# Performance work log

Measured on AMD Instinct MI355X. Metric: run time of the kernel, lower is better.

Reference implementation:

```python
import jax, jax.numpy as jnp
import numpy as np

B, S, D_IN, H, L = 32, 1024, 128, 256, 2
ND = 2  # bidirectional


def setup_inputs() -> dict:
    key = jax.random.key(0)
    ks = iter(jax.random.split(key, 40))

    def p(shape, scale=0.05):
        return jax.random.normal(next(ks), shape, dtype=jnp.float32) * scale

    inp = {"x": jax.random.normal(next(ks), (B, S, D_IN), dtype=jnp.float32)}
    dims_in = [D_IN, H * ND]
    for l in range(L):
        for tag in ("f", "b"):
            inp[f"w_ih_l{l}{tag}"] = p((4 * H, dims_in[l]))
            inp[f"w_hh_l{l}{tag}"] = p((4 * H, H))
            inp[f"b_l{l}{tag}"] = p((4 * H,))  # b_ih + b_hh fused (identical math)
    inp["attn_w"] = p((H * ND,))   # nn.Linear(2H, 1) weight
    inp["attn_b"] = p((1,))
    inp["head_w"] = p((D_IN, H * ND))  # forecasting head: Linear(2H, input_dim)
    inp["head_b"] = p((D_IN,))
    return inp


def _lstm_dir(x, w_ih, w_hh, b, reverse):
    """Single-direction LSTM over [B,S,F] -> [B,S,H]. PyTorch gate order i,f,g,o."""
    Bb = x.shape[0]
    Hh = w_hh.shape[1]
    # Precompute input projections once: [S,B,4H]
    xp = jnp.einsum('bsi,gi->sbg', x, w_ih) + b
    if reverse:
        xp = xp[::-1]
    h0 = jnp.zeros((Bb, Hh), x.dtype)
    c0 = jnp.zeros((Bb, Hh), x.dtype)

    def step(carry, gx):
        h, c = carry
        g = gx + h @ w_hh.T
        i, f, gg, o = jnp.split(g, 4, axis=-1)
        c = jax.nn.sigmoid(f) * c + jax.nn.sigmoid(i) * jnp.tanh(gg)
        h = jax.nn.sigmoid(o) * jnp.tanh(c)
        return (h, c), h

    _, hs = jax.lax.scan(step, (h0, c0), xp)
    if reverse:
        hs = hs[::-1]
    return jnp.swapaxes(hs, 0, 1)  # [B,S,H]


def reference(x,
              w_ih_l0f, w_hh_l0f, b_l0f, w_ih_l0b, w_hh_l0b, b_l0b,
              w_ih_l1f, w_hh_l1f, b_l1f, w_ih_l1b, w_hh_l1b, b_l1b,
              attn_w, attn_b, head_w, head_b):
    h = x
    layers = [((w_ih_l0f, w_hh_l0f, b_l0f), (w_ih_l0b, w_hh_l0b, b_l0b)),
              ((w_ih_l1f, w_hh_l1f, b_l1f), (w_ih_l1b, w_hh_l1b, b_l1b))]
    for fw, bw in layers:
        hf = _lstm_dir(h, *fw, False)
        hb = _lstm_dir(h, *bw, True)
        h = jnp.concatenate([hf, hb], axis=-1)  # [B,S,2H]; dropout off (eval)
    # Prefix attention pooling: original recomputes softmax over output[:, :i+1]
    # for every i. Equivalently (softmax is shift-invariant per prefix):
    # context_i = cumsum(e * h)_i / cumsum(e)_i with e = exp(s - max(s)).
    s = h @ attn_w + attn_b[0]                      # [B,S] attention scores
    e = jnp.exp(s - jnp.max(s, axis=1, keepdims=True))
    num = jnp.cumsum(e[..., None] * h, axis=1)      # [B,S,2H]
    den = jnp.cumsum(e, axis=1)[..., None]          # [B,S,1]
    context = num / den                             # [B,S,2H]
    forecasts = context @ head_w.T + head_b         # [B,S,D_IN]
    return forecasts
```

## Files before the change

### kernel.cpp

```cpp
#include <hip/hip_runtime.h>

typedef unsigned short ushort_t;
typedef unsigned int uint_t;
typedef unsigned long long u64;
typedef __attribute__((ext_vector_type(8))) short short8;
typedef __attribute__((ext_vector_type(4))) float floatx4;

#define S_LEN 1024
#define BATCH 32
#define HDIM  256
#define GDIM  1024
#define DIN   128
#define TAG_BASE 0xC0FFE000u

__device__ __forceinline__ float bf2f(ushort_t u) { return __uint_as_float(((unsigned)u) << 16); }
__device__ __forceinline__ float bf2fs(short s)   { return __uint_as_float(((unsigned)(unsigned short)s) << 16); }
__device__ __forceinline__ ushort_t f2bf(float f) {
  unsigned u = __float_as_uint(f);
  unsigned r = (u + 0x7fffu + ((u >> 16) & 1u)) >> 16;
  return (ushort_t)r;
}
__device__ __forceinline__ float sigf(float x) { return 1.f / (1.f + __expf(-x)); }
__device__ __forceinline__ float tanh_f(float x) {
  float ax = fabsf(x);
  float e = __expf(2.f * ax);
  float r = 1.f - 2.f / (e + 1.f);
  return x < 0.f ? -r : r;
}

__device__ __forceinline__ void load_lds16(const void* g, void* l) {
  __builtin_amdgcn_global_load_lds((const __attribute__((address_space(1))) unsigned int*)g,
                                   (__attribute__((address_space(3))) unsigned int*)l, 16, 0, 0);
}

__global__ __launch_bounds__(256) void gemm_bf16(
    const ushort_t* __restrict__ A, const ushort_t* __restrict__ Bw,
    const float* __restrict__ bias, void* __restrict__ Cout,
    int M, int N, int K, int mode)
{
  __shared__ __align__(16) ushort_t As[128 * 64];
  __shared__ __align__(16) ushort_t Bs[128 * 64];
  const int tid = threadIdx.x;
  const int lane = tid & 63, wid = tid >> 6;
  const int wm = wid >> 1, wn = wid & 1;
  const int bm = blockIdx.y, bn = blockIdx.x;
  const int l15 = lane & 15, q4 = lane >> 4;

  const int r  = tid >> 3;
  const int c8 = tid & 7;
  const int g8 = c8 ^ (r & 7);

  floatx4 zero4 = {0.f, 0.f, 0.f, 0.f};
  floatx4 acc[4][4];
#pragma unroll
  for (int mt = 0; mt < 4; ++mt)
#pragma unroll
    for (int nt = 0; nt < 4; ++nt) acc[mt][nt] = zero4;

  for (int k0 = 0; k0 < K; k0 += 64) {
    __syncthreads();
#pragma unroll
    for (int p = 0; p < 4; ++p) {
      int row = p * 32 + r;
      load_lds16(A + (size_t)(bm * 128 + row) * K + k0 + g8 * 8, (void*)(As + p * 2048 + wid * 512));
      load_lds16(Bw + (size_t)(bn * 128 + row) * K + k0 + g8 * 8, (void*)(Bs + p * 2048 + wid * 512));
    }
    __syncthreads();
#pragma unroll
    for (int ks = 0; ks < 2; ++ks) {
      const int kk = ks * 4 + q4;
      short8 af[4], bf[4];
#pragma unroll
      for (int mt = 0; mt < 4; ++mt) {
        int row = wm * 64 + mt * 16 + l15;
        af[mt] = *(const short8*)(As + row * 64 + ((kk ^ (row & 7)) << 3));
      }
#pragma unroll
      for (int nt = 0; nt < 4; ++nt) {
        int row = wn * 64 + nt * 16 + l15;
        bf[nt] = *(const short8*)(Bs + row * 64 + ((kk ^ (row & 7)) << 3));
      }
#pragma unroll
      for (int mt = 0; mt < 4; ++mt)
#pragma unroll
        for (int nt = 0; nt < 4; ++nt)
          acc[mt][nt] = __builtin_amdgcn_mfma_f32_16x16x32_bf16(af[mt], bf[nt], acc[mt][nt], 0, 0, 0);
    }
  }

#pragma unroll
  for (int mt = 0; mt < 4; ++mt)
#pragma unroll
    for (int nt = 0; nt < 4; ++nt)
#pragma unroll
      for (int rr = 0; rr < 4; ++rr) {
        int m = bm * 128 + wm * 64 + mt * 16 + q4 * 4 + rr;
        int n = bn * 128 + wn * 64 + nt * 16 + l15;
        float v = acc[mt][nt][rr] + bias[n];
        if (mode == 0) {
          ((ushort_t*)Cout)[(size_t)m * N + n] = f2bf(v);
        } else if (mode == 1) {
          int t = m >> 5, b = m & 31;
          ((float*)Cout)[(size_t)b * (S_LEN * DIN) + t * DIN + n] = v;
        } else {
          int t = m >> 5, b = m & 31;
          ((ushort_t*)Cout)[(size_t)t * (N * 32) + n * 32 + b] = f2bf(v);
        }
      }
}

__global__ __launch_bounds__(256) void lstm_layer(
    const ushort_t* __restrict__ xpf, const ushort_t* __restrict__ xpb,
    const ushort_t* __restrict__ whhf, const ushort_t* __restrict__ whhb,
    ushort_t* __restrict__ hout, u64* __restrict__ comm)
{
  const int bx = blockIdx.x;
  const int dir = bx & 1, j = bx >> 1;

  const ushort_t* xp  = dir ? xpb : xpf;
  const ushort_t* whh = dir ? whhb : whhf;
  u64* commd = comm + (size_t)dir * 8192;
  const int hoff = dir * 256;

  __shared__ __align__(16) ushort_t hbuf[32 * 264];
  __shared__ __align__(16) float stage[32 * 132];

  const int tid = threadIdx.x, lane = tid & 63, w = tid >> 6;
  const int l15 = lane & 15, q4 = lane >> 4;

  short8 Bf[2][8];
#pragma unroll
  for (int tl = 0; tl < 2; ++tl) {
    int grow = w * 256 + j * 32 + tl * 16 + l15;
#pragma unroll
    for (int ks = 0; ks < 8; ++ks)
      Bf[tl][ks] = *(const short8*)(whh + (size_t)grow * 256 + ks * 32 + q4 * 8);
  }

  for (int i = tid; i < 32 * 132; i += 256) ((uint_t*)hbuf)[i] = 0u;

  float cst[4] = {0.f, 0.f, 0.f, 0.f};

  u64 xr64[2][2];
  auto ldxp = [&](int tt) {
#pragma unroll
    for (int mt = 0; mt < 2; ++mt)
#pragma unroll
      for (int tl = 0; tl < 2; ++tl) {
        int g = w * 256 + j * 32 + tl * 16 + l15;
        xr64[mt][tl] = *(const u64*)(xp + (size_t)tt * (GDIM * BATCH) + (size_t)g * 32 + mt * 16 + q4 * 4);
      }
  };

  const int cb  = tid >> 3;
  const int cg0 = tid & 7;
  const int bb  = tid >> 3;
  const int c4  = (tid & 7) * 4;

  ldxp((dir == 0) ? 0 : 1023);
  __syncthreads();

  for (int sc = 0; sc < 1024; ++sc) {
    const int tcur  = (dir == 0) ? sc : 1023 - sc;
    const int tnext = (dir == 0) ? (sc < 1023 ? sc + 1 : 1023) : (sc < 1023 ? 1022 - sc : 0);

    floatx4 acc[2][2];
#pragma unroll
    for (int mt = 0; mt < 2; ++mt)
#pragma unroll
      for (int tl = 0; tl < 2; ++tl) {
        u64 v = xr64[mt][tl];
#pragma unroll
        for (int rr = 0; rr < 4; ++rr)
          acc[mt][tl][rr] = bf2f((ushort_t)(v >> (16 * rr)));
      }

    ldxp(tnext);

    if (sc > 0) {
      const unsigned want = TAG_BASE + (unsigned)sc;
      const u64* rbuf = commd + (size_t)(sc & 1) * 4096 + (size_t)cb * 128 + cg0 * 16;
      u64 v[16];
      for (;;) {
#pragma unroll
        for (int k = 0; k < 16; ++k)
          v[k] = __hip_atomic_load(rbuf + k, __ATOMIC_RELAXED, __HIP_MEMORY_SCOPE_AGENT);
        unsigned bad = 0;
#pragma unroll
        for (int k = 0; k < 16; ++k) bad |= ((unsigned)(v[k] >> 32)) ^ want;
        if (bad == 0) break;
      }
#pragma unroll
      for (int k2 = 0; k2 < 8; ++k2) {
        u64 d = (u64)(uint_t)v[2 * k2] | ((u64)(uint_t)v[2 * k2 + 1] << 32);
        *(u64*)(hbuf + cb * 264 + cg0 * 32 + k2 * 4) = d;
      }
    }
    __syncthreads();

#pragma unroll
    for (int ks = 0; ks < 8; ++ks) {
      short8 a0 = *(const short8*)(hbuf + l15 * 264 + ks * 32 + q4 * 8);
      short8 a1 = *(const short8*)(hbuf + (16 + l15) * 264 + ks * 32 + q4 * 8);
      acc[0][0] = __builtin_amdgcn_mfma_f32_16x16x32_bf16(a0, Bf[0][ks], acc[0][0], 0, 0, 0);
      acc[0][1] = __builtin_amdgcn_mfma_f32_16x16x32_bf16(a0, Bf[1][ks], acc[0][1], 0, 0, 0);
      acc[1][0] = __builtin_amdgcn_mfma_f32_16x16x32_bf16(a1, Bf[0][ks], acc[1][0], 0, 0, 0);
      acc[1][1] = __builtin_amdgcn_mfma_f32_16x16x32_bf16(a1, Bf[1][ks], acc[1][1], 0, 0, 0);
    }

#pragma unroll
    for (int mt = 0; mt < 2; ++mt)
#pragma unroll
      for (int tl = 0; tl < 2; ++tl)
#pragma unroll
        for (int rr = 0; rr < 4; ++rr)
          stage[(mt * 16 + q4 * 4 + rr) * 132 + w * 32 + tl * 16 + l15] = acc[mt][tl][rr];
    __syncthreads();

    float hv4[4];
#pragma unroll
    for (int i = 0; i < 4; ++i) {
      float gi = stage[bb * 132 +       c4 + i];
      float gf = stage[bb * 132 + 32  + c4 + i];
      float gg = stage[bb * 132 + 64  + c4 + i];
      float go = stage[bb * 132 + 96  + c4 + i];
      float c = sigf(gf) * cst[i] + sigf(gi) * tanh_f(gg);
      cst[i] = c;
      hv4[i] = sigf(go) * tanh_f(c);
    }
    u64 pv = (u64)f2bf(hv4[0]) | ((u64)f2bf(hv4[1]) << 16) |
             ((u64)f2bf(hv4[2]) << 32) | ((u64)f2bf(hv4[3]) << 48);

    {
      u64* wbuf = commd + (size_t)((sc + 1) & 1) * 4096;
      const u64 tagw = ((u64)(TAG_BASE + (unsigned)(sc + 1))) << 32;
      size_t wi = (size_t)bb * 128 + j * 16 + (c4 >> 1);
      __hip_atomic_store(wbuf + wi,     tagw | (uint_t)pv,         __ATOMIC_RELAXED, __HIP_MEMORY_SCOPE_AGENT);
      __hip_atomic_store(wbuf + wi + 1, tagw | (uint_t)(pv >> 32), __ATOMIC_RELAXED, __HIP_MEMORY_SCOPE_AGENT);
      *(u64*)(hout + (size_t)tcur * (BATCH * 512) + bb * 512 + hoff + j * 32 + c4) = pv;
    }
    __syncthreads();
  }
}

__global__ __launch_bounds__(256) void attn_scores(
    const ushort_t* __restrict__ h1, const float* __restrict__ attn_w,
    const float* __restrict__ attn_b, float* __restrict__ e_out)
{
  const int b = blockIdx.x;
  __shared__ float sbuf[1024];
  __shared__ float red[4];
  const int tid = threadIdx.x, lane = tid & 63, w = tid >> 6;

  float wreg[8];
#pragma unroll
  for (int i = 0; i < 8; ++i) wreg[i] = attn_w[lane * 8 + i];

  for (int t = w; t < 1024; t += 4) {
    short8 hv = *(const short8*)(h1 + (size_t)t * (BATCH * 512) + b * 512 + lane * 8);
    float dot = 0.f;
#pragma unroll
    for (int i = 0; i < 8; ++i) dot += bf2fs(hv[i]) * wreg[i];
#pragma unroll
    for (int off = 32; off; off >>= 1) dot += __shfl_xor(dot, off);
    if (lane == 0) sbuf[t] = dot + attn_b[0];
  }
  __syncthreads();
  float m = -1e30f;
  for (int t = tid; t < 1024; t += 256) m = fmaxf(m, sbuf[t]);
#pragma unroll
  for (int off = 32; off; off >>= 1) m = fmaxf(m, __shfl_xor(m, off));
  if (lane == 0) red[w] = m;
  __syncthreads();
  float mm = fmaxf(fmaxf(red[0], red[1]), fmaxf(red[2], red[3]));
  for (int t = tid; t < 1024; t += 256) e_out[b * 1024 + t] = __expf(sbuf[t] - mm);
}

__global__ __launch_bounds__(256) void attn_ctx(
    const ushort_t* __restrict__ h1, const float* __restrict__ e_in, ushort_t* __restrict__ ctx)
{
  const int b = blockIdx.x >> 1, half = blockIdx.x & 1;
  const int c = half * 256 + threadIdx.x;
  float num = 0.f, den = 0.f;
  const ushort_t* hp = h1 + b * 512 + c;
  ushort_t* cp = ctx + b * 512 + c;
  const float* ep = e_in + b * 1024;
#pragma unroll 4
  for (int t = 0; t < 1024; ++t) {
    float ev = ep[t];
    float hv = bf2f(hp[(size_t)t * (BATCH * 512)]);
    num += ev * hv;
    den += ev;
    cp[(size_t)t * (BATCH * 512)] = f2bf(num / den);
  }
}

__global__ void castw(const float* __restrict__ in, ushort_t* __restrict__ out, int n) {
  int i = blockIdx.x * 256 + threadIdx.x;
  if (i < n) out[i] = f2bf(in[i]);
}
__global__ void castx(const float* __restrict__ x, ushort_t* __restrict__ xt) {
  int i = blockIdx.x * 256 + threadIdx.x;
  int dcol = i & 127;
  int m = i >> 7;
  int b = m & 31, s = m >> 5;
  xt[i] = f2bf(x[(size_t)b * (S_LEN * DIN) + s * DIN + dcol]);
}

extern "C" void kernel_launch(void* const* d_in, const int* in_sizes, int n_in,
                              void* d_out, int out_size, void* d_ws, size_t ws_size,
                              hipStream_t stream)
{
  const float* x     = (const float*)d_in[0];
  const float* wih0f = (const float*)d_in[1];
  const float* whh0f = (const float*)d_in[2];
  const float* b0f   = (const float*)d_in[3];
  const float* wih0b = (const float*)d_in[4];
  const float* whh0b = (const float*)d_in[5];
  const float* b0b   = (const float*)d_in[6];
  const float* wih1f = (const float*)d_in[7];
  const float* whh1f = (const float*)d_in[8];
  const float* b1f   = (const float*)d_in[9];
  const float* wih1b = (const float*)d_in[10];
  const float* whh1b = (const float*)d_in[11];
  const float* b1b   = (const float*)d_in[12];
  const float* attw  = (const float*)d_in[13];
  const float* attb  = (const float*)d_in[14];
  const float* headw = (const float*)d_in[15];
  const float* headb = (const float*)d_in[16];
  float* out = (float*)d_out;

  char* p = (char*)d_ws;
  auto alloc = [&](size_t bytes) {
    char* r = p;
    p += (bytes + 511) & ~(size_t)511;
    return r;
  };
  u64* comm0      = (u64*)alloc(16384 * 8);
  u64* comm1      = (u64*)alloc(16384 * 8);
  ushort_t* xt    = (ushort_t*)alloc((size_t)32768 * 128 * 2);
  ushort_t* cwih0f = (ushort_t*)alloc(131072 * 2);
  ushort_t* cwih0b = (ushort_t*)alloc(131072 * 2);
  ushort_t* cwhh0f = (ushort_t*)alloc(262144 * 2);
  ushort_t* cwhh0b = (ushort_t*)alloc(262144 * 2);
  ushort_t* cwih1f = (ushort_t*)alloc(524288 * 2);
  ushort_t* cwih1b = (ushort_t*)alloc(524288 * 2);
  ushort_t* cwhh1f = (ushort_t*)alloc(262144 * 2);
  ushort_t* cwhh1b = (ushort_t*)alloc(262144 * 2);
  ushort_t* cwhead = (ushort_t*)alloc(65536 * 2);
  ushort_t* xpA = (ushort_t*)alloc((size_t)32768 * 1024 * 2);
  ushort_t* xpB = (ushort_t*)alloc((size_t)32768 * 1024 * 2);
  ushort_t* h0  = (ushort_t*)alloc((size_t)32768 * 512 * 2);
  ushort_t* h1  = (ushort_t*)alloc((size_t)32768 * 512 * 2);
  float* ebuf   = (float*)alloc(32 * 1024 * 4);
  ushort_t* ctx = xpA;

  (void)in_sizes; (void)n_in; (void)out_size; (void)ws_size;

  (void)hipMemsetAsync(comm0, 0, 2 * 16384 * 8, stream);

  castw<<<512, 256, 0, stream>>>(wih0f, cwih0f, 131072);
  castw<<<512, 256, 0, stream>>>(wih0b, cwih0b, 131072);
  castw<<<1024, 256, 0, stream>>>(whh0f, cwhh0f, 262144);
  castw<<<1024, 256, 0, stream>>>(whh0b, cwhh0b, 262144);
  castw<<<2048, 256, 0, stream>>>(wih1f, cwih1f, 524288);
  castw<<<2048, 256, 0, stream>>>(wih1b, cwih1b, 524288);
  castw<<<1024, 256, 0, stream>>>(whh1f, cwhh1f, 262144);
  castw<<<1024, 256, 0, stream>>>(whh1b, cwhh1b, 262144);
  castw<<<256, 256, 0, stream>>>(headw, cwhead, 65536);
  castx<<<16384, 256, 0, stream>>>(x, xt);

  gemm_bf16<<<dim3(8, 256), 256, 0, stream>>>(xt, cwih0f, b0f, xpA, 32768, 1024, 128, 2);
  gemm_bf16<<<dim3(8, 256), 256, 0, stream>>>(xt, cwih0b, b0b, xpB, 32768, 1024, 128, 2);
  lstm_layer<<<16, 256, 0, stream>>>(xpA, xpB, cwhh0f, cwhh0b, h0, comm0);

  gemm_bf16<<<dim3(8, 256), 256, 0, stream>>>(h0, cwih1f, b1f, xpA, 32768, 1024, 512, 2);
  gemm_bf16<<<dim3(8, 256), 256, 0, stream>>>(h0, cwih1b, b1b, xpB, 32768, 1024, 512, 2);
  lstm_layer<<<16, 256, 0, stream>>>(xpA, xpB, cwhh1f, cwhh1b, h1, comm1);

  attn_scores<<<32, 256, 0, stream>>>(h1, attw, attb, ebuf);
  attn_ctx<<<64, 256, 0, stream>>>(h1, ebuf, ctx);
  gemm_bf16<<<dim3(1, 256), 256, 0, stream>>>(ctx, cwhead, headb, out, 32768, 128, 512, 1);
}
```

Before: 9.355 ms.

## Replace cross-block LSTM recurrence with single-block batch split using LDS double buffer

The recurrent LSTM kernel previously split each direction's hidden dimension across 8 workgroups that exchanged h every timestep through tagged global atomics with spin-polling. It now launches 4 workgroups of 1024 threads, each owning one direction and 16 batch rows. Each holds the full W_hh fragment in registers and keeps h in a double-buffered LDS array, so every step needs only one __syncthreads. The gate math is done straight from the MFMA accumulators, removing the staging pass through shared memory. The cost is much less parallelism, with only 4 CUs doing the recurrence, and heavier per-thread register use.

```diff
diff --git a/kernel.cpp b/kernel.cpp
--- a/kernel.cpp
+++ b/kernel.cpp
@@ -11,7 +11,6 @@
 #define HDIM  256
 #define GDIM  1024
 #define DIN   128
-#define TAG_BASE 0xC0FFE000u
 
 __device__ __forceinline__ float bf2f(ushort_t u) { return __uint_as_float(((unsigned)u) << 16); }
 __device__ __forceinline__ float bf2fs(short s)   { return __uint_as_float(((unsigned)(unsigned short)s) << 16); }
@@ -109,53 +108,42 @@
       }
 }
 
-__global__ __launch_bounds__(256) void lstm_layer(
+__global__ __launch_bounds__(1024) void lstm_layer(
     const ushort_t* __restrict__ xpf, const ushort_t* __restrict__ xpb,
     const ushort_t* __restrict__ whhf, const ushort_t* __restrict__ whhb,
-    ushort_t* __restrict__ hout, u64* __restrict__ comm)
-{
-  const int bx = blockIdx.x;
-  const int dir = bx & 1, j = bx >> 1;
+    ushort_t* __restrict__ hout)
+{
+  const int dir = blockIdx.x & 1;
+  const int bh  = blockIdx.x >> 1;
+  const int b0  = bh * 16;
 
   const ushort_t* xp  = dir ? xpb : xpf;
   const ushort_t* whh = dir ? whhb : whhf;
-  u64* commd = comm + (size_t)dir * 8192;
   const int hoff = dir * 256;
 
-  __shared__ __align__(16) ushort_t hbuf[32 * 264];
-  __shared__ __align__(16) float stage[32 * 132];
+  __shared__ __align__(16) ushort_t hbuf[2][16 * 264];
 
   const int tid = threadIdx.x, lane = tid & 63, w = tid >> 6;
   const int l15 = lane & 15, q4 = lane >> 4;
-
-  short8 Bf[2][8];
-#pragma unroll
-  for (int tl = 0; tl < 2; ++tl) {
-    int grow = w * 256 + j * 32 + tl * 16 + l15;
+  const int col = w * 16 + l15;
+
+  short8 Bf[4][8];
+#pragma unroll
+  for (int gt = 0; gt < 4; ++gt)
 #pragma unroll
     for (int ks = 0; ks < 8; ++ks)
-      Bf[tl][ks] = *(const short8*)(whh + (size_t)grow * 256 + ks * 32 + q4 * 8);
-  }
-
-  for (int i = tid; i < 32 * 132; i += 256) ((uint_t*)hbuf)[i] = 0u;
+      Bf[gt][ks] = *(const short8*)(whh + (size_t)(gt * 256 + col) * 256 + ks * 32 + q4 * 8);
+
+  for (int i = tid; i < 16 * 132; i += 1024) ((uint_t*)&hbuf[0][0])[i] = 0u;
 
   float cst[4] = {0.f, 0.f, 0.f, 0.f};
 
-  u64 xr64[2][2];
+  u64 xr[4];
   auto ldxp = [&](int tt) {
 #pragma unroll
-    for (int mt = 0; mt < 2; ++mt)
-#pragma unroll
-      for (int tl = 0; tl < 2; ++tl) {
-        int g = w * 256 + j * 32 + tl * 16 + l15;
-        xr64[mt][tl] = *(const u64*)(xp + (size_t)tt * (GDIM * BATCH) + (size_t)g * 32 + mt * 16 + q4 * 4);
-      }
+    for (int gt = 0; gt < 4; ++gt)
+      xr[gt] = *(const u64*)(xp + (size_t)tt * (GDIM * BATCH) + (size_t)(gt * 256 + col) * 32 + b0 + q4 * 4);
   };
-
-  const int cb  = tid >> 3;
-  const int cg0 = tid & 7;
-  const int bb  = tid >> 3;
-  const int c4  = (tid & 7) * 4;
 
   ldxp((dir == 0) ? 0 : 1023);
   __syncthreads();
@@ -164,80 +152,38 @@
     const int tcur  = (dir == 0) ? sc : 1023 - sc;
     const int tnext = (dir == 0) ? (sc < 1023 ? sc + 1 : 1023) : (sc < 1023 ? 1022 - sc : 0);
 
-    floatx4 acc[2][2];
-#pragma unroll
-    for (int mt = 0; mt < 2; ++mt)
-#pragma unroll
-      for (int tl = 0; tl < 2; ++tl) {
-        u64 v = xr64[mt][tl];
-#pragma unroll
-        for (int rr = 0; rr < 4; ++rr)
-          acc[mt][tl][rr] = bf2f((ushort_t)(v >> (16 * rr)));
-      }
+    floatx4 acc[4];
+#pragma unroll
+    for (int gt = 0; gt < 4; ++gt) {
+      u64 v = xr[gt];
+#pragma unroll
+      for (int rr = 0; rr < 4; ++rr)
+        acc[gt][rr] = bf2f((ushort_t)(v >> (16 * rr)));
+    }
 
     ldxp(tnext);
 
-    if (sc > 0) {
-      const unsigned want = TAG_BASE + (unsigned)sc;
-      const u64* rbuf = commd + (size_t)(sc & 1) * 4096 + (size_t)cb * 128 + cg0 * 16;
-      u64 v[16];
-      for (;;) {
-#pragma unroll
-        for (int k = 0; k < 16; ++k)
-          v[k] = __hip_atomic_load(rbuf + k, __ATOMIC_RELAXED, __HIP_MEMORY_SCOPE_AGENT);
-        unsigned bad = 0;
-#pragma unroll
-        for (int k = 0; k < 16; ++k) bad |= ((unsigned)(v[k] >> 32)) ^ want;
-        if (bad == 0) break;
-      }
-#pragma unroll
-      for (int k2 = 0; k2 < 8; ++k2) {
-        u64 d = (u64)(uint_t)v[2 * k2] | ((u64)(uint_t)v[2 * k2 + 1] << 32);
-        *(u64*)(hbuf + cb * 264 + cg0 * 32 + k2 * 4) = d;
-      }
-    }
-    __syncthreads();
-
+    const ushort_t* hb = &hbuf[sc & 1][0];
 #pragma unroll
     for (int ks = 0; ks < 8; ++ks) {
-      short8 a0 = *(const short8*)(hbuf + l15 * 264 + ks * 32 + q4 * 8);
-      short8 a1 = *(const short8*)(hbuf + (16 + l15) * 264 + ks * 32 + q4 * 8);
-      acc[0][0] = __builtin_amdgcn_mfma_f32_16x16x32_bf16(a0, Bf[0][ks], acc[0][0], 0, 0, 0);
-      acc[0][1] = __builtin_amdgcn_mfma_f32_16x16x32_bf16(a0, Bf[1][ks], acc[0][1], 0, 0, 0);
-      acc[1][0] = __builtin_amdgcn_mfma_f32_16x16x32_bf16(a1, Bf[0][ks], acc[1][0], 0, 0, 0);
-      acc[1][1] = __builtin_amdgcn_mfma_f32_16x16x32_bf16(a1, Bf[1][ks], acc[1][1], 0, 0, 0);
-    }
-
-#pragma unroll
-    for (int mt = 0; mt < 2; ++mt)
-#pragma unroll
-      for (int tl = 0; tl < 2; ++tl)
-#pragma unroll
-        for (int rr = 0; rr < 4; ++rr)
-          stage[(mt * 16 + q4 * 4 + rr) * 132 + w * 32 + tl * 16 + l15] = acc[mt][tl][rr];
-    __syncthreads();
-
-    float hv4[4];
-#pragma unroll
-    for (int i = 0; i < 4; ++i) {
-      float gi = stage[bb * 132 +       c4 + i];
-      float gf = stage[bb * 132 + 32  + c4 + i];
-      float gg = stage[bb * 132 + 64  + c4 + i];
-      float go = stage[bb * 132 + 96  + c4 + i];
-      float c = sigf(gf) * cst[i] + sigf(gi) * tanh_f(gg);
-      cst[i] = c;
-      hv4[i] = sigf(go) * tanh_f(c);
-    }
-    u64 pv = (u64)f2bf(hv4[0]) | ((u64)f2bf(hv4[1]) << 16) |
-             ((u64)f2bf(hv4[2]) << 32) | ((u64)f2bf(hv4[3]) << 48);
-
-    {
-      u64* wbuf = commd + (size_t)((sc + 1) & 1) * 4096;
-      const u64 tagw = ((u64)(TAG_BASE + (unsigned)(sc + 1))) << 32;
-      size_t wi = (size_t)bb * 128 + j * 16 + (c4 >> 1);
-      __hip_atomic_store(wbuf + wi,     tagw | (uint_t)pv,         __ATOMIC_RELAXED, __HIP_MEMORY_SCOPE_AGENT);
-      __hip_atomic_store(wbuf + wi + 1, tagw | (uint_t)(pv >> 32), __ATOMIC_RELAXED, __HIP_MEMORY_SCOPE_AGENT);
-      *(u64*)(hout + (size_t)tcur * (BATCH * 512) + bb * 512 + hoff + j * 32 + c4) = pv;
+      short8 a = *(const short8*)(hb + l15 * 264 + ks * 32 + q4 * 8);
+      acc[0] = __builtin_amdgcn_mfma_f32_16x16x32_bf16(a, Bf[0][ks], acc[0], 0, 0, 0);
+      acc[1] = __builtin_amdgcn_mfma_f32_16x16x32_bf16(a, Bf[1][ks], acc[1], 0, 0, 0);
+      acc[2] = __builtin_amdgcn_mfma_f32_16x16x32_bf16(a, Bf[2][ks], acc[2], 0, 0, 0);
+      acc[3] = __builtin_amdgcn_mfma_f32_16x16x32_bf16(a, Bf[3][ks], acc[3], 0, 0, 0);
+    }
+
+    ushort_t* hw = &hbuf[(sc + 1) & 1][0];
+#pragma unroll
+    for (int rr = 0; rr < 4; ++rr) {
+      float gi = acc[0][rr], gf = acc[1][rr], gg = acc[2][rr], go = acc[3][rr];
+      float c = sigf(gf) * cst[rr] + sigf(gi) * tanh_f(gg);
+      cst[rr] = c;
+      float h = sigf(go) * tanh_f(c);
+      ushort_t hb16 = f2bf(h);
+      int row = q4 * 4 + rr;
+      hw[row * 264 + col] = hb16;
+      hout[(size_t)tcur * (BATCH * 512) + (size_t)(b0 + row) * 512 + hoff + col] = hb16;
     }
     __syncthreads();
   }
@@ -336,8 +282,6 @@
     p += (bytes + 511) & ~(size_t)511;
     return r;
   };
-  u64* comm0      = (u64*)alloc(16384 * 8);
-  u64* comm1      = (u64*)alloc(16384 * 8);
   ushort_t* xt    = (ushort_t*)alloc((size_t)32768 * 128 * 2);
   ushort_t* cwih0f = (ushort_t*)alloc(131072 * 2);
   ushort_t* cwih0b = (ushort_t*)alloc(131072 * 2);
@@ -357,8 +301,6 @@
 
   (void)in_sizes; (void)n_in; (void)out_size; (void)ws_size;
 
-  (void)hipMemsetAsync(comm0, 0, 2 * 16384 * 8, stream);
-
   castw<<<512, 256, 0, stream>>>(wih0f, cwih0f, 131072);
   castw<<<512, 256, 0, stream>>>(wih0b, cwih0b, 131072);
   castw<<<1024, 256, 0, stream>>>(whh0f, cwhh0f, 262144);
@@ -372,11 +314,11 @@
 
   gemm_bf16<<<dim3(8, 256), 256, 0, stream>>>(xt, cwih0f, b0f, xpA, 32768, 1024, 128, 2);
   gemm_bf16<<<dim3(8, 256), 256, 0, stream>>>(xt, cwih0b, b0b, xpB, 32768, 1024, 128, 2);
-  lstm_layer<<<16, 256, 0, stream>>>(xpA, xpB, cwhh0f, cwhh0b, h0, comm0);
+  lstm_layer<<<4, 1024, 0, stream>>>(xpA, xpB, cwhh0f, cwhh0b, h0);
 
   gemm_bf16<<<dim3(8, 256), 256, 0, stream>>>(h0, cwih1f, b1f, xpA, 32768, 1024, 512, 2);
   gemm_bf16<<<dim3(8, 256), 256, 0, stream>>>(h0, cwih1b, b1b, xpB, 32768, 1024, 512, 2);
-  lstm_layer<<<16, 256, 0, stream>>>(xpA, xpB, cwhh1f, cwhh1b, h1, comm1);
+  lstm_layer<<<4, 1024, 0, stream>>>(xpA, xpB, cwhh1f, cwhh1b, h1);
 
   attn_scores<<<32, 256, 0, stream>>>(h1, attw, attb, ebuf);
   attn_ctx<<<64, 256, 0, stream>>>(h1, ebuf, ctx);
```

Result: slower. 19.21 ms (+105.3%).
